# Kernel tuning notes

Measured on AMD Instinct MI355X. Metric: run time of the kernel, lower is better.

## Reference

```python
import jax, jax.numpy as jnp
import numpy as np

B = 65536
IMG = 9            # input spatial size; conv 2x2 valid -> 8x8 = 64 features
RBF_IN = 64
RBF_OUT = 16
HID = 32
GAMMA = 1.0
THRESHOLD = 0.0


def setup_inputs() -> dict:
    key = jax.random.key(0)
    ks = jax.random.split(key, 8)
    x = jax.random.normal(ks[0], (B, 1, IMG, IMG), dtype=jnp.float32)
    conv_w = jax.random.normal(ks[1], (1, 1, 2, 2), dtype=jnp.float32) * 0.5
    conv_b = jax.random.normal(ks[2], (1,), dtype=jnp.float32) * 0.1
    centers = jax.random.normal(ks[3], (RBF_OUT, RBF_IN), dtype=jnp.float32)
    w1 = jax.random.normal(ks[4], (RBF_OUT, HID), dtype=jnp.float32) * (1.0 / np.sqrt(RBF_OUT))
    b1 = jnp.zeros((HID,), dtype=jnp.float32)
    w2 = jax.random.normal(ks[5], (HID, 1), dtype=jnp.float32) * (1.0 / np.sqrt(HID))
    b2 = jnp.zeros((1,), dtype=jnp.float32)
    return {"x": x, "conv_w": conv_w, "conv_b": conv_b, "centers": centers,
            "w1": w1, "b1": b1, "w2": w2, "b2": b2}


def reference(x, conv_w, conv_b, centers, w1, b1, w2, b2):
    # ConvFilter: 2x2 valid conv + bias, sigmoid(logits - threshold)
    logits = jax.lax.conv_general_dilated(
        x, conv_w, window_strides=(1, 1), padding="VALID",
        dimension_numbers=("NCHW", "OIHW", "NCHW"))
    logits = logits + conv_b[None, :, None, None]
    act = jax.nn.sigmoid(logits - THRESHOLD)          # [B,1,8,8]
    flat = act.reshape(act.shape[0], -1)               # [B,64]
    # RBFLayer: exp(-gamma * ||x - c||^2), broadcast diff [B,16,64]
    diff = flat[:, None, :] - centers[None, :, :]
    dist_sq = jnp.sum(diff * diff, axis=-1)            # [B,16]
    rbf = jnp.exp(-GAMMA * dist_sq)
    # Classifier: Linear(16,32) -> tanh -> Linear(32,1) -> sigmoid -> squeeze
    h = jnp.tanh(rbf @ w1 + b1)
    out = jax.nn.sigmoid(h @ w2 + b2)
    return out.squeeze(-1)                              # [B]
```

## Files before the change

kernel.cpp:

```cpp
#include <hip/hip_runtime.h>


constexpr int NPIX    = 81;
constexpr int RBF_IN  = 64;
constexpr int RBF_OUT = 16;
constexpr int HID     = 32;
constexpr int SPB     = 128;

__device__ __forceinline__ float sigmoid_f(float v) {
    return __builtin_amdgcn_rcpf(1.0f + __expf(-v));
}

__device__ __forceinline__ float tanh_f(float v) {
    float vc = fminf(fmaxf(v, -15.0f), 15.0f);
    float e  = __expf(2.0f * vc);
    return (e - 1.0f) * __builtin_amdgcn_rcpf(e + 1.0f);
}

__global__ __launch_bounds__(SPB, 1) void qcnn_fused(
    const float* __restrict__ x,
    const float* __restrict__ conv_w,
    const float* __restrict__ conv_b,
    const float* __restrict__ centers,
    const float* __restrict__ w1,
    const float* __restrict__ b1,
    const float* __restrict__ w2,
    const float* __restrict__ b2,
    float* __restrict__ out,
    int nB)
{
    __shared__ float s_x[SPB * NPIX];
    __shared__ float s_c2t[RBF_IN * RBF_OUT];
    __shared__ float s_cc[RBF_OUT];
    __shared__ float s_w1t[HID * RBF_OUT];
    __shared__ float s_b1[HID];
    __shared__ float s_w2[HID];

    const int tid = threadIdx.x;

    {
        const size_t base  = (size_t)blockIdx.x * (SPB * NPIX);
        const size_t total = (size_t)nB * NPIX;
        if (base + (size_t)(SPB * NPIX) <= total) {
            const float4* __restrict__ xv = (const float4*)(x + base);
            float4* sv = (float4*)s_x;
            #pragma unroll
            for (int i = 0; i < (SPB * NPIX / 4) / SPB; ++i)
                sv[i * SPB + tid] = xv[i * SPB + tid];
            {
                int i = 20 * SPB + tid;
                if (i < SPB * NPIX / 4) sv[i] = xv[i];
            }
        } else {
            for (int i = tid; i < SPB * NPIX; i += SPB) {
                size_t g = base + i;
                s_x[i] = (g < total) ? x[g] : 0.0f;
            }
        }
    }

    for (int idx = tid; idx < RBF_IN * RBF_OUT; idx += SPB) {
        int k = idx >> 4, j = idx & 15;
        s_c2t[idx] = -2.0f * centers[j * RBF_IN + k];
    }
    for (int idx = tid; idx < HID * RBF_OUT; idx += SPB) {
        int i = idx >> 4, j = idx & 15;
        s_w1t[idx] = w1[j * HID + i];
    }
    if (tid < HID) { s_b1[tid] = b1[tid]; s_w2[tid] = w2[tid]; }
    if (tid < RBF_OUT) {
        float s = 0.0f;
        for (int k = 0; k < RBF_IN; ++k) {
            float c = centers[tid * RBF_IN + k];
            s = fmaf(c, c, s);
        }
        s_cc[tid] = s;
    }
    __syncthreads();

    const int b = blockIdx.x * SPB + tid;
    if (b >= nB) return;

    const float w00 = conv_w[0], w01 = conv_w[1], w10 = conv_w[2], w11 = conv_w[3];
    const float cbias = conv_b[0];

    const float* __restrict__ row = &s_x[tid * NPIX];
    float xr[NPIX];
    #pragma unroll
    for (int i = 0; i < NPIX; ++i) xr[i] = row[i];

    float dot[RBF_OUT];
    #pragma unroll
    for (int j = 0; j < RBF_OUT; ++j) dot[j] = 0.0f;
    float S2 = 0.0f;

    #pragma unroll
    for (int r = 0; r < 8; ++r) {
        #pragma unroll
        for (int c = 0; c < 8; ++c) {
            float v = cbias;
            v = fmaf(w00, xr[r*9 + c],      v);
            v = fmaf(w01, xr[r*9 + c + 1],  v);
            v = fmaf(w10, xr[r*9 + 9 + c],  v);
            v = fmaf(w11, xr[r*9 + 10 + c], v);
            float a = sigmoid_f(v);
            S2 = fmaf(a, a, S2);
            const int k = r*8 + c;
            #pragma unroll
            for (int j = 0; j < RBF_OUT; ++j)
                dot[j] = fmaf(a, s_c2t[k*RBF_OUT + j], dot[j]);
        }
    }

    float rbf[RBF_OUT];
    #pragma unroll
    for (int j = 0; j < RBF_OUT; ++j)
        rbf[j] = __expf(-(S2 + dot[j] + s_cc[j]));

    float acc = b2[0];
    #pragma unroll
    for (int i = 0; i < HID; ++i) {
        float hv = s_b1[i];
        #pragma unroll
        for (int j = 0; j < RBF_OUT; ++j)
            hv = fmaf(rbf[j], s_w1t[i*RBF_OUT + j], hv);
        acc = fmaf(tanh_f(hv), s_w2[i], acc);
    }
    out[b] = sigmoid_f(acc);
}

extern "C" void kernel_launch(void* const* d_in, const int* in_sizes, int n_in,
                              void* d_out, int out_size, void* d_ws, size_t ws_size,
                              hipStream_t stream) {
    const float* x       = (const float*)d_in[0];
    const float* conv_w  = (const float*)d_in[1];
    const float* conv_b  = (const float*)d_in[2];
    const float* centers = (const float*)d_in[3];
    const float* w1      = (const float*)d_in[4];
    const float* b1      = (const float*)d_in[5];
    const float* w2      = (const float*)d_in[6];
    const float* b2      = (const float*)d_in[7];
    float* out = (float*)d_out;

    int nB = out_size;
    int grid = (nB + SPB - 1) / SPB;
    qcnn_fused<<<grid, SPB, 0, stream>>>(x, conv_w, conv_b, centers,
                                         w1, b1, w2, b2, out, nB);
}
```

Baseline: 90.60 us.

## Split each sample across two threads with shuffle reductions

Each sample is now processed by a pair of threads instead of one. Each thread computes half of the conv rows and half of the hidden units, and the partial sums are combined with xor-shuffles. The block size doubles to 256 while each block still covers 128 samples, which gives more waves and fewer registers per thread. In exchange it adds shuffle traffic, and half the threads sit idle on the output store.

```diff
diff --git a/kernel.cpp b/kernel.cpp
--- a/kernel.cpp
+++ b/kernel.cpp
@@ -6,6 +6,7 @@
 constexpr int RBF_OUT = 16;
 constexpr int HID     = 32;
 constexpr int SPB     = 128;
+constexpr int TPB     = 256;
 
 __device__ __forceinline__ float sigmoid_f(float v) {
     return __builtin_amdgcn_rcpf(1.0f + __expf(-v));
@@ -17,7 +18,7 @@
     return (e - 1.0f) * __builtin_amdgcn_rcpf(e + 1.0f);
 }
 
-__global__ __launch_bounds__(SPB, 1) void qcnn_fused(
+__global__ __launch_bounds__(TPB, 1) void qcnn_fused(
     const float* __restrict__ x,
     const float* __restrict__ conv_w,
     const float* __restrict__ conv_b,
@@ -45,25 +46,25 @@
             const float4* __restrict__ xv = (const float4*)(x + base);
             float4* sv = (float4*)s_x;
             #pragma unroll
-            for (int i = 0; i < (SPB * NPIX / 4) / SPB; ++i)
-                sv[i * SPB + tid] = xv[i * SPB + tid];
+            for (int i = 0; i < (SPB * NPIX / 4) / TPB; ++i)
+                sv[i * TPB + tid] = xv[i * TPB + tid];
             {
-                int i = 20 * SPB + tid;
+                int i = 10 * TPB + tid;
                 if (i < SPB * NPIX / 4) sv[i] = xv[i];
             }
         } else {
-            for (int i = tid; i < SPB * NPIX; i += SPB) {
+            for (int i = tid; i < SPB * NPIX; i += TPB) {
                 size_t g = base + i;
                 s_x[i] = (g < total) ? x[g] : 0.0f;
             }
         }
     }
 
-    for (int idx = tid; idx < RBF_IN * RBF_OUT; idx += SPB) {
+    for (int idx = tid; idx < RBF_IN * RBF_OUT; idx += TPB) {
         int k = idx >> 4, j = idx & 15;
         s_c2t[idx] = -2.0f * centers[j * RBF_IN + k];
     }
-    for (int idx = tid; idx < HID * RBF_OUT; idx += SPB) {
+    for (int idx = tid; idx < HID * RBF_OUT; idx += TPB) {
         int i = idx >> 4, j = idx & 15;
         s_w1t[idx] = w1[j * HID + i];
     }
@@ -78,24 +79,26 @@
     }
     __syncthreads();
 
-    const int b = blockIdx.x * SPB + tid;
+    const int pair = tid >> 1;
+    const int p    = tid & 1;
+    const int b    = blockIdx.x * SPB + pair;
     if (b >= nB) return;
 
     const float w00 = conv_w[0], w01 = conv_w[1], w10 = conv_w[2], w11 = conv_w[3];
     const float cbias = conv_b[0];
 
-    const float* __restrict__ row = &s_x[tid * NPIX];
-    float xr[NPIX];
+    const float* __restrict__ row = &s_x[pair * NPIX + p * 36];
+    float xr[45];
     #pragma unroll
-    for (int i = 0; i < NPIX; ++i) xr[i] = row[i];
+    for (int i = 0; i < 45; ++i) xr[i] = row[i];
 
-    float dot[RBF_OUT];
+    float dotH[RBF_OUT];
     #pragma unroll
-    for (int j = 0; j < RBF_OUT; ++j) dot[j] = 0.0f;
-    float S2 = 0.0f;
+    for (int j = 0; j < RBF_OUT; ++j) dotH[j] = 0.0f;
+    float S2h = 0.0f;
 
     #pragma unroll
-    for (int r = 0; r < 8; ++r) {
+    for (int r = 0; r < 4; ++r) {
         #pragma unroll
         for (int c = 0; c < 8; ++c) {
             float v = cbias;
@@ -104,29 +107,34 @@
             v = fmaf(w10, xr[r*9 + 9 + c],  v);
             v = fmaf(w11, xr[r*9 + 10 + c], v);
             float a = sigmoid_f(v);
-            S2 = fmaf(a, a, S2);
-            const int k = r*8 + c;
+            S2h = fmaf(a, a, S2h);
+            const int k = (4*p + r)*8 + c;
             #pragma unroll
             for (int j = 0; j < RBF_OUT; ++j)
-                dot[j] = fmaf(a, s_c2t[k*RBF_OUT + j], dot[j]);
+                dotH[j] = fmaf(a, s_c2t[k*RBF_OUT + j], dotH[j]);
         }
     }
 
+    float S2 = S2h + __shfl_xor(S2h, 1);
     float rbf[RBF_OUT];
     #pragma unroll
-    for (int j = 0; j < RBF_OUT; ++j)
-        rbf[j] = __expf(-(S2 + dot[j] + s_cc[j]));
+    for (int j = 0; j < RBF_OUT; ++j) {
+        float d = dotH[j] + __shfl_xor(dotH[j], 1);
+        rbf[j] = __expf(-(S2 + d + s_cc[j]));
+    }
 
-    float acc = b2[0];
+    float accH = 0.0f;
     #pragma unroll
-    for (int i = 0; i < HID; ++i) {
+    for (int m = 0; m < HID/2; ++m) {
+        const int i = 2*m + p;
         float hv = s_b1[i];
         #pragma unroll
         for (int j = 0; j < RBF_OUT; ++j)
             hv = fmaf(rbf[j], s_w1t[i*RBF_OUT + j], hv);
-        acc = fmaf(tanh_f(hv), s_w2[i], acc);
+        accH = fmaf(tanh_f(hv), s_w2[i], accH);
     }
-    out[b] = sigmoid_f(acc);
+    float acc = accH + __shfl_xor(accH, 1) + b2[0];
+    if (p == 0) out[b] = sigmoid_f(acc);
 }
 
 extern "C" void kernel_launch(void* const* d_in, const int* in_sizes, int n_in,
@@ -144,6 +152,6 @@
 
     int nB = out_size;
     int grid = (nB + SPB - 1) / SPB;
-    qcnn_fused<<<grid, SPB, 0, stream>>>(x, conv_w, conv_b, centers,
+    qcnn_fused<<<grid, TPB, 0, stream>>>(x, conv_w, conv_b, centers,
                                          w1, b1, w2, b2, out, nB);
 }
```

Result: faster. 85.74 us (-5.4%).
